# Kernel optimization log

Measured on AMD Instinct MI355X. Metric: run time of the kernel, lower is better.

## Reference

```python
import jax, jax.numpy as jnp
import numpy as np

B, T, C, H = 2, 2048, 2048, 16
HD = C // H


def setup_inputs() -> dict:
    key = jax.random.key(0)
    ks = jax.random.split(key, 5)
    s = 0.02  # init scale for weights
    return {
        "x": jax.random.normal(ks[0], (B, T, C), jnp.float32),
        "Wq": jax.random.normal(ks[1], (C, C), jnp.float32) * s,
        "Wk": jax.random.normal(ks[2], (C, C), jnp.float32) * s,
        "Wv": jax.random.normal(ks[3], (C, C), jnp.float32) * s,
        "Wo": jax.random.normal(ks[4], (C, C), jnp.float32) * s,
        "bo": jnp.zeros((C,), jnp.float32),
    }


def _alibi_slopes(n_head):
    # power-of-2 path of _get_alibi_slopes (n_head=16 is a power of 2)
    return jnp.array([1.0 / 2 ** (i + 1) for i in range(n_head)], jnp.float32)


def reference(x, Wq, Wk, Wv, Wo, bo):
    b, t, c = x.shape
    h, hd = H, HD
    scale = 1.0 / np.sqrt(hd)
    # nn.Linear (no bias): y = x @ W.T; split heads -> (B,H,T,HD)
    q = (x @ Wq.T).reshape(b, t, h, hd).transpose(0, 2, 1, 3)
    k = (x @ Wk.T).reshape(b, t, h, hd).transpose(0, 2, 1, 3)
    v = (x @ Wv.T).reshape(b, t, h, hd).transpose(0, 2, 1, 3)
    scores = jnp.einsum("bhtd,bhsd->bhts", q, k) * scale  # (B,H,T,T)
    pos = jnp.arange(t)
    diff = pos[:, None] - pos[None, :]  # (T,T), i-j
    slopes = _alibi_slopes(h)
    bias = slopes[:, None, None] * diff.astype(jnp.float32)  # (H,T,T)
    causal = diff >= 0  # lower-triangular mask
    bias = jnp.where(causal[None, :, :], bias, -jnp.inf)
    scores = scores + bias[None]  # (B,H,T,T)
    attn = jax.nn.softmax(scores, axis=-1)  # dropout = identity (eval mode)
    out = jnp.einsum("bhts,bhsd->bhtd", attn, v)
    out = out.transpose(0, 2, 1, 3).reshape(b, t, c)
    out = out @ Wo.T + bo  # proj_dropout = identity (eval mode)
    return out, attn
```

## Files before the change

kernel.cpp:

```cpp
#include <hip/hip_runtime.h>
#include <hip/hip_bf16.h>

#define DEVINL __device__ __forceinline__

typedef __attribute__((ext_vector_type(8))) short bf16x8;
typedef __attribute__((ext_vector_type(4))) float f32x4;

DEVINL ushort f2bf(float f) {
  unsigned u = __float_as_uint(f);
  u += 0x7fffu + ((u >> 16) & 1u);
  return (ushort)(u >> 16);
}

DEVINL void gl_lds16(const void* g, void* lds) {
  __builtin_amdgcn_global_load_lds(
      (const __attribute__((address_space(1))) void*)g,
      (__attribute__((address_space(3))) void*)lds, 16, 0, 0);
}

DEVINL f32x4 mfma16(bf16x8 a, bf16x8 b, f32x4 c) {
  return __builtin_amdgcn_mfma_f32_16x16x32_bf16(a, b, c, 0, 0, 0);
}

__global__ __launch_bounds__(256) void cast_all_kernel(const float4* __restrict__ x,
                                                       const float4* __restrict__ wq,
                                                       const float4* __restrict__ wk,
                                                       const float4* __restrict__ wv,
                                                       const float4* __restrict__ wo,
                                                       ushort4* __restrict__ xb,
                                                       ushort4* __restrict__ wqb,
                                                       ushort4* __restrict__ wkb,
                                                       ushort4* __restrict__ wvb,
                                                       ushort4* __restrict__ wob) {
  const int blk = (int)blockIdx.x;
  const float4* src;
  ushort4* dst;
  int base;
  if (blk < 2048)      { src = x;  dst = xb;  base = blk; }
  else if (blk < 3072) { src = wq; dst = wqb; base = blk - 2048; }
  else if (blk < 4096) { src = wk; dst = wkb; base = blk - 3072; }
  else if (blk < 5120) { src = wv; dst = wvb; base = blk - 4096; }
  else                 { src = wo; dst = wob; base = blk - 5120; }
  const int idx0 = base * 1024 + (int)threadIdx.x;
#pragma unroll
  for (int i = 0; i < 4; ++i) {
    const int idx = idx0 + i * 256;
    float4 v = src[idx];
    dst[idx] = make_ushort4(f2bf(v.x), f2bf(v.y), f2bf(v.z), f2bf(v.w));
  }
}

template <int MODE>
__global__ __launch_bounds__(256) void gemm_nt(const ushort* __restrict__ A,
                                               const ushort* __restrict__ Bm,
                                               ushort* __restrict__ Qo,
                                               ushort* __restrict__ Ko,
                                               ushort* __restrict__ Vo,
                                               float* __restrict__ Fo,
                                               const float* __restrict__ bias,
                                               int M, int N, int K) {
  __shared__ __align__(16) ushort Al[2][8192];
  __shared__ __align__(16) ushort Bl[2][8192];
  const int tid = (int)threadIdx.x;
  const int l = tid & 63, w = tid >> 6;
  const int wr = w >> 1, wc = w & 1;
  const int lr = l & 15, lg = l >> 4;

  const int nwg = (int)(gridDim.x * gridDim.y);
  const int flat = (int)(blockIdx.y * gridDim.x + blockIdx.x);
  const int swz = (flat & 7) * (nwg >> 3) + (flat >> 3);
  const int bx = swz % (int)gridDim.x, by = swz / (int)gridDim.x;
  const int rowT = by * 128, colT = bx * 128;

  f32x4 acc[4][4] = {};

  auto stage = [&](int kt, int buf) {
#pragma unroll
    for (int q = 0; q < 4; ++q) {
      int s = q * 256 + tid;
      int rb = s >> 7, ks = (s >> 6) & 1, sl = s & 63;
      size_t koff = (size_t)(kt + ks * 32 + (sl >> 4) * 8);
      gl_lds16(A + (size_t)(rowT + rb * 16 + (sl & 15)) * K + koff,
               &Al[buf][(size_t)(q * 256 + (tid & 192)) * 8]);
      gl_lds16(Bm + (size_t)(colT + rb * 16 + (sl & 15)) * K + koff,
               &Bl[buf][(size_t)(q * 256 + (tid & 192)) * 8]);
    }
  };

  stage(0, 0);
  __syncthreads();
  int cur = 0;
  for (int kt = 0; kt < K; kt += 64) {
    if (kt + 64 < K) stage(kt + 64, cur ^ 1);
#pragma unroll
    for (int ks = 0; ks < 2; ++ks) {
      bf16x8 af[4], bfv[4];
#pragma unroll
      for (int i = 0; i < 4; ++i) {
        af[i]  = *(const bf16x8*)(&Al[cur][(((wr * 4 + i) * 2 + ks) * 64 + l) * 8]);
        bfv[i] = *(const bf16x8*)(&Bl[cur][(((wc * 4 + i) * 2 + ks) * 64 + l) * 8]);
      }
#pragma unroll
      for (int i = 0; i < 4; ++i)
#pragma unroll
        for (int j = 0; j < 4; ++j)
          acc[i][j] = mfma16(af[i], bfv[j], acc[i][j]);
    }
    __syncthreads();
    cur ^= 1;
  }

  const int seg = colT >> 11;
#pragma unroll
  for (int i = 0; i < 4; ++i) {
#pragma unroll
    for (int j = 0; j < 4; ++j) {
      const int col = colT + wc * 64 + j * 16 + lr;
#pragma unroll
      for (int e = 0; e < 4; ++e) {
        const int row = rowT + wr * 64 + i * 16 + lg * 4 + e;
        float v = acc[i][j][e];
        if (MODE == 3) {
          const int c = col & 2047;
          if (seg == 0)      Qo[(size_t)row * 2048 + c] = f2bf(v);
          else if (seg == 1) Ko[(size_t)row * 2048 + c] = f2bf(v);
          else               Vo[((size_t)((row >> 11) * 2048 + c)) * 2048 + (row & 2047)] = f2bf(v);
        } else {
          __builtin_nontemporal_store(v + bias[col], &Fo[(size_t)row * 2048 + col]);
        }
      }
    }
  }
}

__global__ __launch_bounds__(256) void flash_kernel(const ushort* __restrict__ Qg,
                                                    const ushort* __restrict__ Kg,
                                                    const ushort* __restrict__ Vt,
                                                    ushort* __restrict__ Og,
                                                    float2* __restrict__ stats) {
  __shared__ __align__(16) ushort Kl[2][8192];
  __shared__ __align__(16) ushort Vl[2][8192];
  __shared__ __align__(16) ushort Pl[4][1024];

  const int flat = (int)(blockIdx.y * gridDim.x + blockIdx.x);
  const int swz = (flat & 7) * 64 + (flat >> 3);
  const int bx = swz & 15, bh = swz >> 4;
  const int b = bh >> 4, h = bh & 15;
  const int tid = (int)threadIdx.x, l = tid & 63, w = tid >> 6;
  const int lr = l & 15, lg = l >> 4;
  const float scale = 0.08838834764831845f;
  const float slope = exp2f(-(float)(h + 1));
  const ushort* Kbase = Kg + ((size_t)b * 2048) * 2048 + h * 128;
  const ushort* Vbase = Vt + ((size_t)b * 2048 + h * 128) * 2048;

  for (int half = 0; half < 2; ++half) {
    const int qb = (half == 0) ? 31 - bx : bx;
    const int qr0 = qb * 64 + w * 16;

    bf16x8 qf[4];
#pragma unroll
    for (int ks = 0; ks < 4; ++ks)
      qf[ks] = *(const bf16x8*)(Qg + ((size_t)b * 2048 + qr0 + lr) * 2048 + h * 128 + ks * 32 + lg * 8);

    float runmax[4], runsum[4];
    f32x4 o[8] = {};
#pragma unroll
    for (int j = 0; j < 4; ++j) { runmax[j] = -__builtin_inff(); runsum[j] = 0.f; }

    auto stage = [&](int jt, int buf) {
#pragma unroll
      for (int q = 0; q < 4; ++q) {
        const int s = q * 256 + tid;
        const int sl = s & 63;
        const int cb = s >> 8, ks = (s >> 6) & 3;
        gl_lds16(Kbase + (size_t)(jt * 64 + cb * 16 + (sl & 15)) * 2048 + ks * 32 + (sl >> 4) * 8,
                 &Kl[buf][(size_t)(q * 256 + (tid & 192)) * 8]);
        const int db = s >> 7, k2 = (s >> 6) & 1;
        gl_lds16(Vbase + (size_t)(db * 16 + (sl & 15)) * 2048 + jt * 64 + k2 * 32 + (sl >> 4) * 8,
                 &Vl[buf][(size_t)(q * 256 + (tid & 192)) * 8]);
      }
    };

    stage(qb, 0);
    __syncthreads();

    for (int jt = qb; jt >= 0; --jt) {
      const int cur = (qb - jt) & 1;
      if (jt > 0) stage(jt - 1, cur ^ 1);

      f32x4 sc[4];
      __builtin_amdgcn_s_setprio(1);
#pragma unroll
      for (int cb = 0; cb < 4; ++cb) {
        f32x4 a = {};
#pragma unroll
        for (int ks = 0; ks < 4; ++ks) {
          bf16x8 kf = *(const bf16x8*)(&Kl[cur][((cb * 4 + ks) * 64 + l) * 8]);
          a = mfma16(qf[ks], kf, a);
        }
        sc[cb] = a;
      }
      __builtin_amdgcn_s_setprio(0);
#pragma unroll
      for (int cb = 0; cb < 4; ++cb) {
        const int kj = jt * 64 + cb * 16 + lr;
#pragma unroll
        for (int j = 0; j < 4; ++j) {
          const int qi = qr0 + lg * 4 + j;
          sc[cb][j] = (kj <= qi) ? sc[cb][j] * scale + slope * (float)(qi - kj) : -__builtin_inff();
        }
      }

      float nm[4];
      bool need = false;
#pragma unroll
      for (int j = 0; j < 4; ++j) {
        float m = fmaxf(fmaxf(sc[0][j], sc[1][j]), fmaxf(sc[2][j], sc[3][j]));
#pragma unroll
        for (int d = 1; d < 16; d <<= 1) m = fmaxf(m, __shfl_xor(m, d));
        nm[j] = fmaxf(runmax[j], m);
        need = need || (nm[j] > runmax[j]);
      }
      if (__any(need)) {
#pragma unroll
        for (int j = 0; j < 4; ++j) {
          const float f = __expf(runmax[j] - nm[j]);
          runsum[j] *= f;
#pragma unroll
          for (int db = 0; db < 8; ++db) o[db][j] *= f;
          runmax[j] = nm[j];
        }
      }

#pragma unroll
      for (int cb = 0; cb < 4; ++cb) {
        const int kc = cb * 16 + lr;
#pragma unroll
        for (int j = 0; j < 4; ++j) {
          const float p = __expf(sc[cb][j] - runmax[j]);
          runsum[j] += p;
          const int l2 = (((kc & 31) >> 3) << 4) | (lg * 4 + j);
          Pl[w][((kc >> 5) * 64 + l2) * 8 + (kc & 7)] = f2bf(p);
        }
      }

      bf16x8 pf0 = *(const bf16x8*)(&Pl[w][(size_t)l * 8]);
      bf16x8 pf1 = *(const bf16x8*)(&Pl[w][(size_t)(64 + l) * 8]);
      __builtin_amdgcn_s_setprio(1);
#pragma unroll
      for (int db = 0; db < 8; ++db) {
        o[db] = mfma16(pf0, *(const bf16x8*)(&Vl[cur][((db * 2 + 0) * 64 + l) * 8]), o[db]);
        o[db] = mfma16(pf1, *(const bf16x8*)(&Vl[cur][((db * 2 + 1) * 64 + l) * 8]), o[db]);
      }
      __builtin_amdgcn_s_setprio(0);
      __syncthreads();
    }

#pragma unroll
    for (int j = 0; j < 4; ++j) {
      float s = runsum[j];
#pragma unroll
      for (int d = 1; d < 16; d <<= 1) s += __shfl_xor(s, d);
      const float iv = 1.0f / s;
      if (lr == 0) stats[(size_t)bh * 2048 + qr0 + lg * 4 + j] = make_float2(runmax[j], iv);
#pragma unroll
      for (int db = 0; db < 8; ++db) o[db][j] *= iv;
    }
#pragma unroll
    for (int db = 0; db < 8; ++db)
#pragma unroll
      for (int j = 0; j < 4; ++j)
        Og[((size_t)b * 2048 + qr0 + lg * 4 + j) * 2048 + h * 128 + db * 16 + lr] = f2bf(o[db][j]);
  }
}

__global__ __launch_bounds__(256) void probs_kernel(const ushort* __restrict__ Qg,
                                                    const ushort* __restrict__ Kg,
                                                    const float2* __restrict__ stats,
                                                    float* __restrict__ attn_out) {
  const int kb = (int)blockIdx.x, qb = (int)blockIdx.y, bh = (int)blockIdx.z;
  const int tid = (int)threadIdx.x;

  if (kb > qb) {
    float* base = attn_out + ((size_t)bh * 2048 + qb * 128) * 2048 + kb * 128;
    const f32x4 z = {0.f, 0.f, 0.f, 0.f};
#pragma unroll
    for (int it = 0; it < 16; ++it) {
      const int idx = it * 256 + tid;
      __builtin_nontemporal_store(z, (f32x4*)(base + (size_t)(idx >> 5) * 2048 + (idx & 31) * 4));
    }
    return;
  }

  __shared__ __align__(16) ushort Ql[16384];
  __shared__ __align__(16) ushort Kl[16384];
  const int b = bh >> 4, h = bh & 15;
  const int l = tid & 63, w = tid >> 6;
  const int wr = w >> 1, wc = w & 1;
  const int lr = l & 15, lg = l >> 4;
  const float scale = 0.08838834764831845f;
  const float slope = exp2f(-(float)(h + 1));

#pragma unroll
  for (int q = 0; q < 8; ++q) {
    const int s = q * 256 + tid;
    const int sl = s & 63, rb = s >> 8, ks = (s >> 6) & 3;
    const size_t koff = (size_t)(h * 128 + ks * 32 + (sl >> 4) * 8);
    gl_lds16(Qg + ((size_t)b * 2048 + qb * 128 + rb * 16 + (sl & 15)) * 2048 + koff,
             Ql + (size_t)(q * 256 + (tid & 192)) * 8);
    gl_lds16(Kg + ((size_t)b * 2048 + kb * 128 + rb * 16 + (sl & 15)) * 2048 + koff,
             Kl + (size_t)(q * 256 + (tid & 192)) * 8);
  }
  __syncthreads();

  f32x4 acc[4][4] = {};
#pragma unroll
  for (int ks = 0; ks < 4; ++ks) {
    bf16x8 af[4], bfv[4];
#pragma unroll
    for (int i = 0; i < 4; ++i) {
      af[i]  = *(const bf16x8*)(Ql + (((wr * 4 + i) * 4 + ks) * 64 + l) * 8);
      bfv[i] = *(const bf16x8*)(Kl + (((wc * 4 + i) * 4 + ks) * 64 + l) * 8);
    }
#pragma unroll
    for (int i = 0; i < 4; ++i)
#pragma unroll
      for (int j = 0; j < 4; ++j)
        acc[i][j] = mfma16(af[i], bfv[j], acc[i][j]);
  }

  float2 st[4][4];
#pragma unroll
  for (int i = 0; i < 4; ++i)
#pragma unroll
    for (int e = 0; e < 4; ++e)
      st[i][e] = stats[(size_t)bh * 2048 + qb * 128 + wr * 64 + i * 16 + lg * 4 + e];

#pragma unroll
  for (int i = 0; i < 4; ++i) {
#pragma unroll
    for (int j = 0; j < 4; ++j) {
      const int kj = kb * 128 + wc * 64 + j * 16 + lr;
#pragma unroll
      for (int e = 0; e < 4; ++e) {
        const int qi = qb * 128 + wr * 64 + i * 16 + lg * 4 + e;
        const float sv = acc[i][j][e] * scale + slope * (float)(qi - kj);
        float p = __expf(sv - st[i][e].x) * st[i][e].y;
        if (kj > qi) p = 0.f;
        __builtin_nontemporal_store(p, &attn_out[((size_t)bh * 2048 + qi) * 2048 + kj]);
      }
    }
  }
}

extern "C" void kernel_launch(void* const* d_in, const int* in_sizes, int n_in,
                              void* d_out, int out_size, void* d_ws, size_t ws_size,
                              hipStream_t stream) {
  (void)in_sizes; (void)n_in; (void)out_size; (void)ws_size;
  const float* x  = (const float*)d_in[0];
  const float* Wq = (const float*)d_in[1];
  const float* Wk = (const float*)d_in[2];
  const float* Wv = (const float*)d_in[3];
  const float* Wo = (const float*)d_in[4];
  const float* bo = (const float*)d_in[5];

  float* outp  = (float*)d_out;
  float* attnp = outp + (size_t)4096 * 2048;

  char* ws = (char*)d_ws;
  ushort* xb   = (ushort*)(ws);
  ushort* wqkv = (ushort*)(ws + (16ull << 20));
  ushort* wob  = (ushort*)(ws + (40ull << 20));
  ushort* Qb   = (ushort*)(ws + (48ull << 20));
  ushort* Kb   = (ushort*)(ws + (64ull << 20));
  ushort* Vtb  = (ushort*)(ws + (80ull << 20));
  ushort* Ob   = (ushort*)(ws + (96ull << 20));
  float2* stats = (float2*)(ws);

  cast_all_kernel<<<6144, 256, 0, stream>>>(
      (const float4*)x, (const float4*)Wq, (const float4*)Wk, (const float4*)Wv,
      (const float4*)Wo, (ushort4*)xb, (ushort4*)wqkv, (ushort4*)(wqkv + 4194304),
      (ushort4*)(wqkv + 2 * 4194304), (ushort4*)wob);

  gemm_nt<3><<<dim3(48, 32), 256, 0, stream>>>(xb, wqkv, Qb, Kb, Vtb, nullptr, nullptr,
                                               4096, 6144, 2048);

  flash_kernel<<<dim3(16, 32), 256, 0, stream>>>(Qb, Kb, Vtb, Ob, stats);
  probs_kernel<<<dim3(16, 16, 32), 256, 0, stream>>>(Qb, Kb, stats, attnp);

  gemm_nt<2><<<dim3(16, 32), 256, 0, stream>>>(Ob, wob, nullptr, nullptr, nullptr, outp, bo,
                                               4096, 2048, 2048);
}
```

Before: 523.6 us.

## Enlarge GEMM tiles to 256x256 and stage attention probs through LDS

The projection GEMMs move from 128x128 tiles with 4 waves to 256x256 tiles with 8 waves (512 threads), doubling LDS buffers and per-wave accumulators. The aim is more operand reuse per loaded byte. The output-projection GEMM drops to 128 workgroups, which may underfill the GPU and raise register pressure. Separately, the probs kernel writes its tile into a swizzled LDS buffer and then emits coalesced 16-byte nontemporal stores instead of scattered scalar stores to the large attention output.

Measured after the change: 550.8 us. +5.2%, slower.

```diff
diff --git a/kernel.cpp b/kernel.cpp
--- a/kernel.cpp
+++ b/kernel.cpp
@@ -51,39 +51,39 @@
 }
 
 template <int MODE>
-__global__ __launch_bounds__(256) void gemm_nt(const ushort* __restrict__ A,
-                                               const ushort* __restrict__ Bm,
-                                               ushort* __restrict__ Qo,
-                                               ushort* __restrict__ Ko,
-                                               ushort* __restrict__ Vo,
-                                               float* __restrict__ Fo,
-                                               const float* __restrict__ bias,
-                                               int M, int N, int K) {
-  __shared__ __align__(16) ushort Al[2][8192];
-  __shared__ __align__(16) ushort Bl[2][8192];
+__global__ __launch_bounds__(512, 2) void gemm_nt(const ushort* __restrict__ A,
+                                                  const ushort* __restrict__ Bm,
+                                                  ushort* __restrict__ Qo,
+                                                  ushort* __restrict__ Ko,
+                                                  ushort* __restrict__ Vo,
+                                                  float* __restrict__ Fo,
+                                                  const float* __restrict__ bias,
+                                                  int M, int N, int K) {
+  __shared__ __align__(16) ushort Al[2][16384];
+  __shared__ __align__(16) ushort Bl[2][16384];
   const int tid = (int)threadIdx.x;
   const int l = tid & 63, w = tid >> 6;
-  const int wr = w >> 1, wc = w & 1;
+  const int wr = w >> 2, wc = w & 3;
   const int lr = l & 15, lg = l >> 4;
 
   const int nwg = (int)(gridDim.x * gridDim.y);
   const int flat = (int)(blockIdx.y * gridDim.x + blockIdx.x);
   const int swz = (flat & 7) * (nwg >> 3) + (flat >> 3);
   const int bx = swz % (int)gridDim.x, by = swz / (int)gridDim.x;
-  const int rowT = by * 128, colT = bx * 128;
-
-  f32x4 acc[4][4] = {};
+  const int rowT = by * 256, colT = bx * 256;
+
+  f32x4 acc[8][4] = {};
 
   auto stage = [&](int kt, int buf) {
 #pragma unroll
-    for (int q = 0; q < 4; ++q) {
-      int s = q * 256 + tid;
+    for (int r = 0; r < 4; ++r) {
+      int s = r * 512 + tid;
       int rb = s >> 7, ks = (s >> 6) & 1, sl = s & 63;
       size_t koff = (size_t)(kt + ks * 32 + (sl >> 4) * 8);
       gl_lds16(A + (size_t)(rowT + rb * 16 + (sl & 15)) * K + koff,
-               &Al[buf][(size_t)(q * 256 + (tid & 192)) * 8]);
+               &Al[buf][(size_t)(r * 512 + (tid & 448)) * 8]);
       gl_lds16(Bm + (size_t)(colT + rb * 16 + (sl & 15)) * K + koff,
-               &Bl[buf][(size_t)(q * 256 + (tid & 192)) * 8]);
+               &Bl[buf][(size_t)(r * 512 + (tid & 448)) * 8]);
     }
   };
 
@@ -94,14 +94,15 @@
     if (kt + 64 < K) stage(kt + 64, cur ^ 1);
 #pragma unroll
     for (int ks = 0; ks < 2; ++ks) {
-      bf16x8 af[4], bfv[4];
-#pragma unroll
-      for (int i = 0; i < 4; ++i) {
-        af[i]  = *(const bf16x8*)(&Al[cur][(((wr * 4 + i) * 2 + ks) * 64 + l) * 8]);
-        bfv[i] = *(const bf16x8*)(&Bl[cur][(((wc * 4 + i) * 2 + ks) * 64 + l) * 8]);
-      }
-#pragma unroll
-      for (int i = 0; i < 4; ++i)
+      bf16x8 af[8], bfv[4];
+#pragma unroll
+      for (int i = 0; i < 8; ++i)
+        af[i] = *(const bf16x8*)(&Al[cur][(((wr * 8 + i) * 2 + ks) * 64 + l) * 8]);
+#pragma unroll
+      for (int j = 0; j < 4; ++j)
+        bfv[j] = *(const bf16x8*)(&Bl[cur][(((wc * 4 + j) * 2 + ks) * 64 + l) * 8]);
+#pragma unroll
+      for (int i = 0; i < 8; ++i)
 #pragma unroll
         for (int j = 0; j < 4; ++j)
           acc[i][j] = mfma16(af[i], bfv[j], acc[i][j]);
@@ -112,13 +113,13 @@
 
   const int seg = colT >> 11;
 #pragma unroll
-  for (int i = 0; i < 4; ++i) {
+  for (int i = 0; i < 8; ++i) {
 #pragma unroll
     for (int j = 0; j < 4; ++j) {
       const int col = colT + wc * 64 + j * 16 + lr;
 #pragma unroll
       for (int e = 0; e < 4; ++e) {
-        const int row = rowT + wr * 64 + i * 16 + lg * 4 + e;
+        const int row = rowT + wr * 128 + i * 16 + lg * 4 + e;
         float v = acc[i][j][e];
         if (MODE == 3) {
           const int c = col & 2047;
@@ -292,8 +293,10 @@
     return;
   }
 
-  __shared__ __align__(16) ushort Ql[16384];
-  __shared__ __align__(16) ushort Kl[16384];
+  __shared__ __align__(16) ushort SM[32768];
+  ushort* Ql = SM;
+  ushort* Kl = SM + 16384;
+  float* Pf = (float*)SM;
   const int b = bh >> 4, h = bh & 15;
   const int l = tid & 63, w = tid >> 6;
   const int wr = w >> 1, wc = w & 1;
@@ -336,20 +339,34 @@
     for (int e = 0; e < 4; ++e)
       st[i][e] = stats[(size_t)bh * 2048 + qb * 128 + wr * 64 + i * 16 + lg * 4 + e];
 
+  __syncthreads();
+
 #pragma unroll
   for (int i = 0; i < 4; ++i) {
 #pragma unroll
     for (int j = 0; j < 4; ++j) {
-      const int kj = kb * 128 + wc * 64 + j * 16 + lr;
+      const int cl = wc * 64 + j * 16 + lr;
+      const int kj = kb * 128 + cl;
 #pragma unroll
       for (int e = 0; e < 4; ++e) {
-        const int qi = qb * 128 + wr * 64 + i * 16 + lg * 4 + e;
+        const int rl = wr * 64 + i * 16 + lg * 4 + e;
+        const int qi = qb * 128 + rl;
         const float sv = acc[i][j][e] * scale + slope * (float)(qi - kj);
         float p = __expf(sv - st[i][e].x) * st[i][e].y;
         if (kj > qi) p = 0.f;
-        __builtin_nontemporal_store(p, &attn_out[((size_t)bh * 2048 + qi) * 2048 + kj]);
-      }
-    }
+        Pf[rl * 128 + ((cl + (rl << 2)) & 127)] = p;
+      }
+    }
+  }
+  __syncthreads();
+
+  float* gbase = attn_out + ((size_t)bh * 2048 + qb * 128) * 2048 + kb * 128;
+#pragma unroll
+  for (int it = 0; it < 16; ++it) {
+    const int idx = it * 256 + tid;
+    const int row = idx >> 5, c4 = (idx & 31) << 2;
+    f32x4 v = *(const f32x4*)(&Pf[row * 128 + ((c4 + (row << 2)) & 127)]);
+    __builtin_nontemporal_store(v, (f32x4*)(gbase + (size_t)row * 2048 + c4));
   }
 }
 
@@ -382,12 +399,12 @@
       (const float4*)Wo, (ushort4*)xb, (ushort4*)wqkv, (ushort4*)(wqkv + 4194304),
       (ushort4*)(wqkv + 2 * 4194304), (ushort4*)wob);
 
-  gemm_nt<3><<<dim3(48, 32), 256, 0, stream>>>(xb, wqkv, Qb, Kb, Vtb, nullptr, nullptr,
+  gemm_nt<3><<<dim3(24, 16), 512, 0, stream>>>(xb, wqkv, Qb, Kb, Vtb, nullptr, nullptr,
                                                4096, 6144, 2048);
 
   flash_kernel<<<dim3(16, 32), 256, 0, stream>>>(Qb, Kb, Vtb, Ob, stats);
   probs_kernel<<<dim3(16, 16, 32), 256, 0, stream>>>(Qb, Kb, stats, attnp);
 
-  gemm_nt<2><<<dim3(16, 32), 256, 0, stream>>>(Ob, wob, nullptr, nullptr, nullptr, outp, bo,
-                                               4096, 2048, 2048);
-}
+  gemm_nt<2><<<dim3(8, 16), 512, 0, stream>>>(Ob, wob, nullptr, nullptr, nullptr, outp, bo,
+                                              4096, 2048, 2048);
+}
```
